# Kernel tuning notes

Hardware: AMD Instinct MI355X
Metric: run time of the kernel (lower is better)

## Reference

```python
import jax, jax.numpy as jnp
import numpy as np

D_MODEL = 2048
N_HEADS = 16
D_HEAD = D_MODEL // N_HEADS  # 128


def setup_inputs() -> dict:
    key = jax.random.key(0)
    ks = jax.random.split(key, 5)
    b, t = 2, 2048
    s = 0.02
    return {
        "x": jax.random.normal(ks[0], (b, t, D_MODEL), dtype=jnp.float32),
        "Wq": jax.random.normal(ks[1], (D_MODEL, D_MODEL), dtype=jnp.float32) * s,
        "Wk": jax.random.normal(ks[2], (D_MODEL, D_HEAD), dtype=jnp.float32) * s,
        "Wv": jax.random.normal(ks[3], (D_MODEL, D_HEAD), dtype=jnp.float32) * s,
        "Wo": jax.random.normal(ks[4], (D_MODEL, D_MODEL), dtype=jnp.float32) * s,
    }


def reference(x, Wq, Wk, Wv, Wo):
    b, t, c = x.shape
    scale = D_HEAD ** -0.5
    # q: [b, h, t, d]; k, v: single shared KV head [b, s, d]
    q = (x @ Wq).reshape(b, t, N_HEADS, D_HEAD).transpose(0, 2, 1, 3)
    k = x @ Wk  # [b, s, d]
    v = x @ Wv  # [b, s, d]
    # broadcast the shared KV head across query heads without materializing copies
    scores = jnp.einsum('bhtd,bsd->bhts', q, k) * scale
    attn = jax.nn.softmax(scores, axis=-1)
    y = jnp.einsum('bhts,bsd->bhtd', attn, v)
    y = y.transpose(0, 2, 1, 3).reshape(b, t, c)
    return y @ Wo
```

## Files before the change

kernel.cpp:

```cpp
#include <hip/hip_runtime.h>

typedef unsigned short ushort_t;
typedef short bf16x8 __attribute__((ext_vector_type(8)));
typedef float f32x4 __attribute__((ext_vector_type(4)));

#define B_    2
#define T_    2048
#define C_    2048
#define H_    16
#define DH_   128
#define BT_   4096
#define NQKV  2304

#define OFF_XB   0UL
#define OFF_WT   16777216UL
#define OFF_WOT  26214400UL
#define OFF_QKV  34603008UL
#define OFF_VT   53477376UL
#define OFF_FLAG 54525952UL

__device__ __forceinline__ ushort_t f2bf(float f) {
  union { float f; unsigned u; } v; v.f = f;
  unsigned r = v.u + 0x7fffu + ((v.u >> 16) & 1u);
  return (ushort_t)(r >> 16);
}
__device__ __forceinline__ float bf2f(ushort_t u) {
  union { float f; unsigned u; } v; v.u = ((unsigned)u) << 16;
  return v.f;
}
__device__ __forceinline__ int cvtpk_bf16(float lo, float hi) {
  int r;
  asm("v_cvt_pk_bf16_f32 %0, %1, %2" : "=v"(r) : "v"(lo), "v"(hi));
  return r;
}
__device__ __forceinline__ bf16x8 mkfrag(int d0, int d1, int d2, int d3) {
  union { int i[4]; bf16x8 v; } u;
  u.i[0] = d0; u.i[1] = d1; u.i[2] = d2; u.i[3] = d3;
  return u.v;
}

__device__ __forceinline__ void gload_lds16(const ushort_t* g, ushort_t* l) {
  __builtin_amdgcn_global_load_lds((__attribute__((address_space(1))) void*)g,
                                   (__attribute__((address_space(3))) void*)l,
                                   16, 0, 0);
}

__global__ void detect_dtype(const ushort_t* x, int* flag) {
  if (threadIdx.x == 0 && blockIdx.x == 0) {
    int sane = 0;
    for (int i = 0; i < 32; ++i) {
      ushort_t u = x[2 * i];
      int e = (u >> 7) & 0xFF;
      if (u == 0 || (e >= 100 && e <= 140)) ++sane;
    }
    *flag = (sane >= 24) ? 1 : 0;
  }
}

__global__ __launch_bounds__(256) void cast_x(const void* __restrict__ xin,
                                              ushort_t* __restrict__ xb,
                                              const int* __restrict__ flag, int n8) {
  int i = blockIdx.x * 256 + threadIdx.x;
  if (i >= n8) return;
  if (*flag) {
    *(bf16x8*)(xb + (size_t)i * 8) = *(const bf16x8*)((const ushort_t*)xin + (size_t)i * 8);
  } else {
    const float* xf = (const float*)xin;
    f32x4 a = *(const f32x4*)(xf + (size_t)i * 8);
    f32x4 b = *(const f32x4*)(xf + (size_t)i * 8 + 4);
    bf16x8 o;
    o[0] = (short)f2bf(a[0]); o[1] = (short)f2bf(a[1]);
    o[2] = (short)f2bf(a[2]); o[3] = (short)f2bf(a[3]);
    o[4] = (short)f2bf(b[0]); o[5] = (short)f2bf(b[1]);
    o[6] = (short)f2bf(b[2]); o[7] = (short)f2bf(b[3]);
    *(bf16x8*)(xb + (size_t)i * 8) = o;
  }
}

__global__ __launch_bounds__(256) void transpose_cast(const void* __restrict__ src,
                                                      ushort_t* __restrict__ dst,
                                                      const int* __restrict__ flag,
                                                      int rows, int cols, int dst_ld,
                                                      int dst_row_off) {
  __shared__ float tile[32][33];
  int c0 = blockIdx.x * 32, r0 = blockIdx.y * 32;
  int tx = threadIdx.x & 31, ty = threadIdx.x >> 5;
  bool isbf = (*flag != 0);
#pragma unroll
  for (int j = 0; j < 4; ++j) {
    int r = r0 + ty + j * 8;
    float v;
    if (isbf) v = bf2f(((const ushort_t*)src)[(size_t)r * cols + c0 + tx]);
    else      v = ((const float*)src)[(size_t)r * cols + c0 + tx];
    tile[ty + j * 8][tx] = v;
  }
  __syncthreads();
#pragma unroll
  for (int j = 0; j < 4; ++j) {
    int c = c0 + ty + j * 8;
    dst[(size_t)(dst_row_off + c) * dst_ld + r0 + tx] = f2bf(tile[tx][ty + j * 8]);
  }
}

__global__ __launch_bounds__(256) void transpose_v(const ushort_t* __restrict__ qkv,
                                                   ushort_t* __restrict__ vT) {
  __shared__ ushort_t tile[32][33];
  int b = blockIdx.z;
  int t0 = blockIdx.x * 32, d0 = blockIdx.y * 32;
  int tx = threadIdx.x & 31, ty = threadIdx.x >> 5;
#pragma unroll
  for (int j = 0; j < 4; ++j) {
    int t = t0 + ty + j * 8;
    tile[ty + j * 8][tx] = qkv[(size_t)(b * T_ + t) * NQKV + 2176 + d0 + tx];
  }
  __syncthreads();
#pragma unroll
  for (int j = 0; j < 4; ++j) {
    int d = d0 + ty + j * 8;
    vT[(size_t)b * (DH_ * T_) + (size_t)d * T_ + t0 + tx] = tile[tx][ty + j * 8];
  }
}

__global__ __launch_bounds__(256) void gemm_bt(const ushort_t* __restrict__ A,
                                               const ushort_t* __restrict__ Bt,
                                               void* __restrict__ Cv,
                                               int M, int N, int K,
                                               int is_final, const int* __restrict__ flag,
                                               float qscale, int qcols) {
  __shared__ __align__(16) ushort_t As[128 * 32];
  __shared__ __align__(16) ushort_t Bs[128 * 32];
  const int tid = threadIdx.x;
  const int lane = tid & 63;
  const int wid = tid >> 6;
  const int m0 = blockIdx.y * 128;
  const int n0 = blockIdx.x * 128;
  const int wr = wid >> 1, wc = wid & 1;
  const int l15 = lane & 15, l4 = lane >> 4;

  f32x4 zero = {0.f, 0.f, 0.f, 0.f};
  f32x4 acc[4][4];
#pragma unroll
  for (int r = 0; r < 4; ++r)
#pragma unroll
    for (int c = 0; c < 4; ++c) acc[r][c] = zero;

  const ushort_t* ga = A + (size_t)(m0 + (tid >> 2)) * K + (tid & 3) * 8;
  const ushort_t* gb = Bt + (size_t)(n0 + (tid >> 2)) * K + (tid & 3) * 8;
  ushort_t* lA = As + wid * 512;
  ushort_t* lB = Bs + wid * 512;
  const size_t stride64 = (size_t)64 * K;

  for (int k0 = 0; k0 < K; k0 += 32) {
    __syncthreads();
    gload_lds16(ga + k0, lA);
    gload_lds16(ga + k0 + stride64, lA + 2048);
    gload_lds16(gb + k0, lB);
    gload_lds16(gb + k0 + stride64, lB + 2048);
    __syncthreads();

    bf16x8 af[4], bfr[4];
#pragma unroll
    for (int r = 0; r < 4; ++r)
      af[r] = *(const bf16x8*)&As[(wr * 64 + r * 16 + l15) * 32 + l4 * 8];
#pragma unroll
    for (int c = 0; c < 4; ++c)
      bfr[c] = *(const bf16x8*)&Bs[(wc * 64 + c * 16 + l15) * 32 + l4 * 8];
#pragma unroll
    for (int r = 0; r < 4; ++r)
#pragma unroll
      for (int c = 0; c < 4; ++c)
        acc[r][c] = __builtin_amdgcn_mfma_f32_16x16x32_bf16(af[r], bfr[c], acc[r][c], 0, 0, 0);
  }

  const bool f32out = is_final && (*flag == 0);
#pragma unroll
  for (int r = 0; r < 4; ++r) {
#pragma unroll
    for (int c = 0; c < 4; ++c) {
      int row = m0 + wr * 64 + r * 16 + l4 * 4;
      int col = n0 + wc * 64 + c * 16 + l15;
      float s = (col < qcols) ? qscale : 1.0f;
#pragma unroll
      for (int g = 0; g < 4; ++g) {
        float v = acc[r][c][g] * s;
        if (f32out) ((float*)Cv)[(size_t)(row + g) * N + col] = v;
        else ((ushort_t*)Cv)[(size_t)(row + g) * N + col] = f2bf(v);
      }
    }
  }
}

__global__ __launch_bounds__(512, 4) void attn_kernel(const ushort_t* __restrict__ qkv,
                                                      const ushort_t* __restrict__ vT,
                                                      ushort_t* __restrict__ y) {
  __shared__ __align__(16) ushort_t Ks[2][64 * 128];
  __shared__ __align__(16) ushort_t Vs[2][128 * 64];

  const int tid = threadIdx.x;
  const int lane = tid & 63;
  const int wid = tid >> 6;
  const int h = blockIdx.y * 2 + (wid >> 2);
  const int b = blockIdx.z;
  const int tb = b * T_;
  const int q0 = blockIdx.x * 64 + (wid & 3) * 16;
  const int l15 = lane & 15, l4 = lane >> 4;

  bf16x8 qf[4];
  {
    const ushort_t* qbase = qkv + (size_t)(tb + q0 + l15) * NQKV + h * DH_ + l4 * 8;
#pragma unroll
    for (int ks = 0; ks < 4; ++ks) qf[ks] = *(const bf16x8*)(qbase + ks * 32);
  }

  const ushort_t* ksrcb[2];
  const ushort_t* vsrcb[2];
  int koff[2], voff[2];
#pragma unroll
  for (int it = 0; it < 2; ++it) {
    int id = tid + it * 512;
    int krow = id >> 4, kslot = id & 15;
    ksrcb[it] = qkv + (size_t)(tb + krow) * NQKV + 2048 + ((kslot ^ (krow & 7)) << 3);
    int vrow = id >> 3, vslot = id & 7;
    vsrcb[it] = vT + (size_t)b * (DH_ * T_) + (size_t)vrow * T_ + ((vslot ^ (vrow & 7)) << 3);
    koff[it] = (it * 512 + (wid << 6)) * 8;
    voff[it] = (it * 512 + (wid << 6)) * 8;
  }

  f32x4 zero = {0.f, 0.f, 0.f, 0.f};
  f32x4 o[8];
#pragma unroll
  for (int i = 0; i < 8; ++i) o[i] = zero;
  float m_s = -1e30f;
  float l_s = 0.f;

#pragma unroll
  for (int it = 0; it < 2; ++it) {
    gload_lds16(ksrcb[it], &Ks[0][koff[it]]);
    gload_lds16(vsrcb[it], &Vs[0][voff[it]]);
  }

  for (int st = 0; st < 32; ++st) {
    const int cur = st & 1;
    __syncthreads();
    if (st < 31) {
      const int s1 = (st + 1) * 64;
#pragma unroll
      for (int it = 0; it < 2; ++it) {
        gload_lds16(ksrcb[it] + (size_t)s1 * NQKV, &Ks[cur ^ 1][koff[it]]);
        gload_lds16(vsrcb[it] + s1, &Vs[cur ^ 1][voff[it]]);
      }
    }

    f32x4 sa[4];
#pragma unroll
    for (int c = 0; c < 4; ++c) {
      sa[c] = zero;
      int srow = c * 16 + l15;
      int sw = srow & 7;
#pragma unroll
      for (int ks = 0; ks < 4; ++ks) {
        bf16x8 kf = *(const bf16x8*)&Ks[cur][srow * 128 + (((ks * 4 + l4) ^ sw) << 3)];
        sa[c] = __builtin_amdgcn_mfma_f32_16x16x32_bf16(kf, qf[ks], sa[c], 0, 0, 0);
      }
    }

    float pmax = sa[0][0];
#pragma unroll
    for (int c = 0; c < 4; ++c)
#pragma unroll
      for (int r = 0; r < 4; ++r) pmax = fmaxf(pmax, sa[c][r]);
    pmax = fmaxf(pmax, __shfl_xor(pmax, 16));
    pmax = fmaxf(pmax, __shfl_xor(pmax, 32));

    if (!__all(pmax - m_s <= 8.0f)) {
      float mn = fmaxf(m_s, pmax);
      float al = exp2f(m_s - mn);
      m_s = mn;
      l_s *= al;
      float ar[4];
#pragma unroll
      for (int r = 0; r < 4; ++r) ar[r] = __shfl(al, l4 * 4 + r);
#pragma unroll
      for (int nb = 0; nb < 8; ++nb)
#pragma unroll
        for (int r = 0; r < 4; ++r) o[nb][r] *= ar[r];
    }

    float ps = 0.f;
#pragma unroll
    for (int c = 0; c < 4; ++c)
#pragma unroll
      for (int r = 0; r < 4; ++r) {
        float p = exp2f(sa[c][r] - m_s);
        sa[c][r] = p;
        ps += p;
      }
    ps += __shfl_xor(ps, 16);
    ps += __shfl_xor(ps, 32);
    l_s += ps;

    int pk0[2], pk1[2], pk2[2], pk3[2];
    pk0[0] = cvtpk_bf16(sa[0][0], sa[0][1]); pk0[1] = cvtpk_bf16(sa[0][2], sa[0][3]);
    pk1[0] = cvtpk_bf16(sa[1][0], sa[1][1]); pk1[1] = cvtpk_bf16(sa[1][2], sa[1][3]);
    pk2[0] = cvtpk_bf16(sa[2][0], sa[2][1]); pk2[1] = cvtpk_bf16(sa[2][2], sa[2][3]);
    pk3[0] = cvtpk_bf16(sa[3][0], sa[3][1]); pk3[1] = cvtpk_bf16(sa[3][2], sa[3][3]);

    const int srcA = ((lane >> 4) & 1) * 32 + l15;
    const int srcB = srcA + 16;
    const bool cHi = lane >= 32;

    int a00 = __shfl(pk0[0], srcA), a01 = __shfl(pk0[1], srcA);
    int a02 = __shfl(pk0[0], srcB), a03 = __shfl(pk0[1], srcB);
    int b00 = __shfl(pk1[0], srcA), b01 = __shfl(pk1[1], srcA);
    int b02 = __shfl(pk1[0], srcB), b03 = __shfl(pk1[1], srcB);
    bf16x8 pa0 = mkfrag(cHi ? b00 : a00, cHi ? b01 : a01,
                        cHi ? b02 : a02, cHi ? b03 : a03);

    int a10 = __shfl(pk2[0], srcA), a11 = __shfl(pk2[1], srcA);
    int a12 = __shfl(pk2[0], srcB), a13 = __shfl(pk2[1], srcB);
    int b10 = __shfl(pk3[0], srcA), b11 = __shfl(pk3[1], srcA);
    int b12 = __shfl(pk3[0], srcB), b13 = __shfl(pk3[1], srcB);
    bf16x8 pa1 = mkfrag(cHi ? b10 : a10, cHi ? b11 : a11,
                        cHi ? b12 : a12, cHi ? b13 : a13);

#pragma unroll
    for (int nb = 0; nb < 8; ++nb) {
      int vrow = nb * 16 + l15;
      int sw = vrow & 7;
      bf16x8 vb0 = *(const bf16x8*)&Vs[cur][vrow * 64 + ((l4 ^ sw) << 3)];
      o[nb] = __builtin_amdgcn_mfma_f32_16x16x32_bf16(pa0, vb0, o[nb], 0, 0, 0);
      bf16x8 vb1 = *(const bf16x8*)&Vs[cur][vrow * 64 + (((4 + l4) ^ sw) << 3)];
      o[nb] = __builtin_amdgcn_mfma_f32_16x16x32_bf16(pa1, vb1, o[nb], 0, 0, 0);
    }
  }

  float lr[4];
#pragma unroll
  for (int r = 0; r < 4; ++r) lr[r] = __shfl(l_s, l4 * 4 + r);
#pragma unroll
  for (int nb = 0; nb < 8; ++nb) {
#pragma unroll
    for (int r = 0; r < 4; ++r) {
      int qrow = tb + q0 + l4 * 4 + r;
      y[(size_t)qrow * C_ + h * DH_ + nb * 16 + l15] = f2bf(o[nb][r] / lr[r]);
    }
  }
}

extern "C" void kernel_launch(void* const* d_in, const int* in_sizes, int n_in,
                              void* d_out, int out_size, void* d_ws, size_t ws_size,
                              hipStream_t stream) {
  (void)in_sizes; (void)n_in; (void)out_size; (void)ws_size;
  const void* x  = d_in[0];
  const void* Wq = d_in[1];
  const void* Wk = d_in[2];
  const void* Wv = d_in[3];
  const void* Wo = d_in[4];

  char* ws = (char*)d_ws;
  ushort_t* xb  = (ushort_t*)(ws + OFF_XB);
  ushort_t* WT  = (ushort_t*)(ws + OFF_WT);
  ushort_t* WoT = (ushort_t*)(ws + OFF_WOT);
  ushort_t* qkv = (ushort_t*)(ws + OFF_QKV);
  ushort_t* vTp = (ushort_t*)(ws + OFF_VT);
  int* flag     = (int*)(ws + OFF_FLAG);

  detect_dtype<<<1, 1, 0, stream>>>((const ushort_t*)x, flag);

  cast_x<<<4096, 256, 0, stream>>>(x, xb, flag, (BT_ * C_) / 8);

  transpose_cast<<<dim3(64, 64), 256, 0, stream>>>(Wq, WT, flag, 2048, 2048, 2048, 0);
  transpose_cast<<<dim3(4, 64), 256, 0, stream>>>(Wk, WT, flag, 2048, 128, 2048, 2048);
  transpose_cast<<<dim3(4, 64), 256, 0, stream>>>(Wv, WT, flag, 2048, 128, 2048, 2176);
  transpose_cast<<<dim3(64, 64), 256, 0, stream>>>(Wo, WoT, flag, 2048, 2048, 2048, 0);

  const float k1 = 0.08838834764831845f * 1.4426950408889634f;
  gemm_bt<<<dim3(NQKV / 128, BT_ / 128), 256, 0, stream>>>(xb, WT, qkv, BT_, NQKV, C_, 0, flag, k1, 2048);

  transpose_v<<<dim3(T_ / 32, DH_ / 32, B_), 256, 0, stream>>>(qkv, vTp);

  attn_kernel<<<dim3(T_ / 64, H_ / 2, B_), 512, 0, stream>>>(qkv, vTp, xb);

  gemm_bt<<<dim3(C_ / 128, BT_ / 128), 256, 0, stream>>>(xb, WoT, d_out, BT_, C_, C_, 1, flag, 1.0f, 0);
}
```

Baseline: 363.2 us.

## Double-buffer GEMM loads, remap workgroups per XCD, and widen attention query tile

The GEMM now double-buffers its LDS tiles, prefetching the next K-slice while computing the current one with explicit vmcnt waits. It also remaps workgroup IDs so neighbouring tiles land on the same XCD, and raises wave priority around the MFMA blocks. The attention kernel gives each wave 32 query rows in two groups that share each K/V fragment load, halving the grid and the K/V reloads per query. In exchange it raises register pressure, with occupancy lowered to 2, and doubles GEMM LDS use.

```diff
diff --git a/kernel.cpp b/kernel.cpp
--- a/kernel.cpp
+++ b/kernel.cpp
@@ -127,13 +127,22 @@
                                                int M, int N, int K,
                                                int is_final, const int* __restrict__ flag,
                                                float qscale, int qcols) {
-  __shared__ __align__(16) ushort_t As[128 * 32];
-  __shared__ __align__(16) ushort_t Bs[128 * 32];
+  __shared__ __align__(16) ushort_t As[2][128 * 32];
+  __shared__ __align__(16) ushort_t Bs[2][128 * 32];
   const int tid = threadIdx.x;
   const int lane = tid & 63;
   const int wid = tid >> 6;
-  const int m0 = blockIdx.y * 128;
-  const int n0 = blockIdx.x * 128;
+
+  const int gx = gridDim.x;
+  const int nwg = gx * gridDim.y;
+  const int orig = blockIdx.y * gx + blockIdx.x;
+  const int qq = nwg >> 3, rr = nwg & 7;
+  const int xcd = orig & 7, pos = orig >> 3;
+  const int wg = (xcd < rr ? xcd * (qq + 1) : rr * (qq + 1) + (xcd - rr) * qq) + pos;
+  const int bx = wg % gx, by = wg / gx;
+
+  const int m0 = by * 128;
+  const int n0 = bx * 128;
   const int wr = wid >> 1, wc = wid & 1;
   const int l15 = lane & 15, l4 = lane >> 4;
 
@@ -146,30 +155,44 @@
 
   const ushort_t* ga = A + (size_t)(m0 + (tid >> 2)) * K + (tid & 3) * 8;
   const ushort_t* gb = Bt + (size_t)(n0 + (tid >> 2)) * K + (tid & 3) * 8;
-  ushort_t* lA = As + wid * 512;
-  ushort_t* lB = Bs + wid * 512;
   const size_t stride64 = (size_t)64 * K;
-
-  for (int k0 = 0; k0 < K; k0 += 32) {
-    __syncthreads();
-    gload_lds16(ga + k0, lA);
-    gload_lds16(ga + k0 + stride64, lA + 2048);
-    gload_lds16(gb + k0, lB);
-    gload_lds16(gb + k0 + stride64, lB + 2048);
-    __syncthreads();
+  const int lofs = wid * 512;
+
+  gload_lds16(ga, As[0] + lofs);
+  gload_lds16(ga + stride64, As[0] + lofs + 2048);
+  gload_lds16(gb, Bs[0] + lofs);
+  gload_lds16(gb + stride64, Bs[0] + lofs + 2048);
+
+  const int NT = K >> 5;
+  for (int t = 0; t < NT; ++t) {
+    const int cur = t & 1;
+    if (t + 1 < NT) {
+      const int k1 = (t + 1) << 5;
+      gload_lds16(ga + k1, As[cur ^ 1] + lofs);
+      gload_lds16(ga + k1 + stride64, As[cur ^ 1] + lofs + 2048);
+      gload_lds16(gb + k1, Bs[cur ^ 1] + lofs);
+      gload_lds16(gb + k1 + stride64, Bs[cur ^ 1] + lofs + 2048);
+      asm volatile("s_waitcnt vmcnt(4)" ::: "memory");
+    } else {
+      asm volatile("s_waitcnt vmcnt(0)" ::: "memory");
+    }
+    __builtin_amdgcn_s_barrier();
 
     bf16x8 af[4], bfr[4];
 #pragma unroll
     for (int r = 0; r < 4; ++r)
-      af[r] = *(const bf16x8*)&As[(wr * 64 + r * 16 + l15) * 32 + l4 * 8];
+      af[r] = *(const bf16x8*)&As[cur][(wr * 64 + r * 16 + l15) * 32 + l4 * 8];
 #pragma unroll
     for (int c = 0; c < 4; ++c)
-      bfr[c] = *(const bf16x8*)&Bs[(wc * 64 + c * 16 + l15) * 32 + l4 * 8];
+      bfr[c] = *(const bf16x8*)&Bs[cur][(wc * 64 + c * 16 + l15) * 32 + l4 * 8];
+    __builtin_amdgcn_s_setprio(1);
 #pragma unroll
     for (int r = 0; r < 4; ++r)
 #pragma unroll
       for (int c = 0; c < 4; ++c)
         acc[r][c] = __builtin_amdgcn_mfma_f32_16x16x32_bf16(af[r], bfr[c], acc[r][c], 0, 0, 0);
+    __builtin_amdgcn_s_setprio(0);
+    __builtin_amdgcn_s_barrier();
   }
 
   const bool f32out = is_final && (*flag == 0);
@@ -190,7 +213,7 @@
   }
 }
 
-__global__ __launch_bounds__(512, 4) void attn_kernel(const ushort_t* __restrict__ qkv,
+__global__ __launch_bounds__(512, 2) void attn_kernel(const ushort_t* __restrict__ qkv,
                                                       const ushort_t* __restrict__ vT,
                                                       ushort_t* __restrict__ y) {
   __shared__ __align__(16) ushort_t Ks[2][64 * 128];
@@ -202,14 +225,18 @@
   const int h = blockIdx.y * 2 + (wid >> 2);
   const int b = blockIdx.z;
   const int tb = b * T_;
-  const int q0 = blockIdx.x * 64 + (wid & 3) * 16;
+  const int q0 = blockIdx.x * 128 + (wid & 3) * 32;
   const int l15 = lane & 15, l4 = lane >> 4;
 
-  bf16x8 qf[4];
+  bf16x8 qf0[4], qf1[4];
   {
-    const ushort_t* qbase = qkv + (size_t)(tb + q0 + l15) * NQKV + h * DH_ + l4 * 8;
-#pragma unroll
-    for (int ks = 0; ks < 4; ++ks) qf[ks] = *(const bf16x8*)(qbase + ks * 32);
+    const ushort_t* qb0 = qkv + (size_t)(tb + q0 + l15) * NQKV + h * DH_ + l4 * 8;
+    const ushort_t* qb1 = qb0 + (size_t)16 * NQKV;
+#pragma unroll
+    for (int ks = 0; ks < 4; ++ks) {
+      qf0[ks] = *(const bf16x8*)(qb0 + ks * 32);
+      qf1[ks] = *(const bf16x8*)(qb1 + ks * 32);
+    }
   }
 
   const ushort_t* ksrcb[2];
@@ -227,11 +254,11 @@
   }
 
   f32x4 zero = {0.f, 0.f, 0.f, 0.f};
-  f32x4 o[8];
-#pragma unroll
-  for (int i = 0; i < 8; ++i) o[i] = zero;
-  float m_s = -1e30f;
-  float l_s = 0.f;
+  f32x4 o0[8], o1[8];
+#pragma unroll
+  for (int i = 0; i < 8; ++i) { o0[i] = zero; o1[i] = zero; }
+  float m0s = -1e30f, m1s = -1e30f;
+  float l0s = 0.f, l1s = 0.f;
 
 #pragma unroll
   for (int it = 0; it < 2; ++it) {
@@ -251,99 +278,167 @@
       }
     }
 
-    f32x4 sa[4];
+    f32x4 sa0[4], sa1[4];
+    __builtin_amdgcn_s_setprio(1);
 #pragma unroll
     for (int c = 0; c < 4; ++c) {
-      sa[c] = zero;
       int srow = c * 16 + l15;
       int sw = srow & 7;
+      bf16x8 kf[4];
+#pragma unroll
+      for (int ks = 0; ks < 4; ++ks)
+        kf[ks] = *(const bf16x8*)&Ks[cur][srow * 128 + (((ks * 4 + l4) ^ sw) << 3)];
+      sa0[c] = zero; sa1[c] = zero;
 #pragma unroll
       for (int ks = 0; ks < 4; ++ks) {
-        bf16x8 kf = *(const bf16x8*)&Ks[cur][srow * 128 + (((ks * 4 + l4) ^ sw) << 3)];
-        sa[c] = __builtin_amdgcn_mfma_f32_16x16x32_bf16(kf, qf[ks], sa[c], 0, 0, 0);
-      }
-    }
-
-    float pmax = sa[0][0];
+        sa0[c] = __builtin_amdgcn_mfma_f32_16x16x32_bf16(kf[ks], qf0[ks], sa0[c], 0, 0, 0);
+        sa1[c] = __builtin_amdgcn_mfma_f32_16x16x32_bf16(kf[ks], qf1[ks], sa1[c], 0, 0, 0);
+      }
+    }
+    __builtin_amdgcn_s_setprio(0);
+
+    float pmax0 = sa0[0][0];
 #pragma unroll
     for (int c = 0; c < 4; ++c)
 #pragma unroll
-      for (int r = 0; r < 4; ++r) pmax = fmaxf(pmax, sa[c][r]);
-    pmax = fmaxf(pmax, __shfl_xor(pmax, 16));
-    pmax = fmaxf(pmax, __shfl_xor(pmax, 32));
-
-    if (!__all(pmax - m_s <= 8.0f)) {
-      float mn = fmaxf(m_s, pmax);
-      float al = exp2f(m_s - mn);
-      m_s = mn;
-      l_s *= al;
+      for (int r = 0; r < 4; ++r) pmax0 = fmaxf(pmax0, sa0[c][r]);
+    pmax0 = fmaxf(pmax0, __shfl_xor(pmax0, 16));
+    pmax0 = fmaxf(pmax0, __shfl_xor(pmax0, 32));
+    if (!__all(pmax0 - m0s <= 8.0f)) {
+      float mn = fmaxf(m0s, pmax0);
+      float al = exp2f(m0s - mn);
+      m0s = mn; l0s *= al;
       float ar[4];
 #pragma unroll
       for (int r = 0; r < 4; ++r) ar[r] = __shfl(al, l4 * 4 + r);
 #pragma unroll
       for (int nb = 0; nb < 8; ++nb)
 #pragma unroll
-        for (int r = 0; r < 4; ++r) o[nb][r] *= ar[r];
-    }
-
-    float ps = 0.f;
+        for (int r = 0; r < 4; ++r) o0[nb][r] *= ar[r];
+    }
+    float ps0 = 0.f;
 #pragma unroll
     for (int c = 0; c < 4; ++c)
 #pragma unroll
       for (int r = 0; r < 4; ++r) {
-        float p = exp2f(sa[c][r] - m_s);
-        sa[c][r] = p;
-        ps += p;
-      }
-    ps += __shfl_xor(ps, 16);
-    ps += __shfl_xor(ps, 32);
-    l_s += ps;
-
-    int pk0[2], pk1[2], pk2[2], pk3[2];
-    pk0[0] = cvtpk_bf16(sa[0][0], sa[0][1]); pk0[1] = cvtpk_bf16(sa[0][2], sa[0][3]);
-    pk1[0] = cvtpk_bf16(sa[1][0], sa[1][1]); pk1[1] = cvtpk_bf16(sa[1][2], sa[1][3]);
-    pk2[0] = cvtpk_bf16(sa[2][0], sa[2][1]); pk2[1] = cvtpk_bf16(sa[2][2], sa[2][3]);
-    pk3[0] = cvtpk_bf16(sa[3][0], sa[3][1]); pk3[1] = cvtpk_bf16(sa[3][2], sa[3][3]);
+        float p = exp2f(sa0[c][r] - m0s);
+        sa0[c][r] = p;
+        ps0 += p;
+      }
+    ps0 += __shfl_xor(ps0, 16);
+    ps0 += __shfl_xor(ps0, 32);
+    l0s += ps0;
+
+    float pmax1 = sa1[0][0];
+#pragma unroll
+    for (int c = 0; c < 4; ++c)
+#pragma unroll
+      for (int r = 0; r < 4; ++r) pmax1 = fmaxf(pmax1, sa1[c][r]);
+    pmax1 = fmaxf(pmax1, __shfl_xor(pmax1, 16));
+    pmax1 = fmaxf(pmax1, __shfl_xor(pmax1, 32));
+    if (!__all(pmax1 - m1s <= 8.0f)) {
+      float mn = fmaxf(m1s, pmax1);
+      float al = exp2f(m1s - mn);
+      m1s = mn; l1s *= al;
+      float ar[4];
+#pragma unroll
+      for (int r = 0; r < 4; ++r) ar[r] = __shfl(al, l4 * 4 + r);
+#pragma unroll
+      for (int nb = 0; nb < 8; ++nb)
+#pragma unroll
+        for (int r = 0; r < 4; ++r) o1[nb][r] *= ar[r];
+    }
+    float ps1 = 0.f;
+#pragma unroll
+    for (int c = 0; c < 4; ++c)
+#pragma unroll
+      for (int r = 0; r < 4; ++r) {
+        float p = exp2f(sa1[c][r] - m1s);
+        sa1[c][r] = p;
+        ps1 += p;
+      }
+    ps1 += __shfl_xor(ps1, 16);
+    ps1 += __shfl_xor(ps1, 32);
+    l1s += ps1;
 
     const int srcA = ((lane >> 4) & 1) * 32 + l15;
     const int srcB = srcA + 16;
     const bool cHi = lane >= 32;
 
-    int a00 = __shfl(pk0[0], srcA), a01 = __shfl(pk0[1], srcA);
-    int a02 = __shfl(pk0[0], srcB), a03 = __shfl(pk0[1], srcB);
-    int b00 = __shfl(pk1[0], srcA), b01 = __shfl(pk1[1], srcA);
-    int b02 = __shfl(pk1[0], srcB), b03 = __shfl(pk1[1], srcB);
-    bf16x8 pa0 = mkfrag(cHi ? b00 : a00, cHi ? b01 : a01,
-                        cHi ? b02 : a02, cHi ? b03 : a03);
-
-    int a10 = __shfl(pk2[0], srcA), a11 = __shfl(pk2[1], srcA);
-    int a12 = __shfl(pk2[0], srcB), a13 = __shfl(pk2[1], srcB);
-    int b10 = __shfl(pk3[0], srcA), b11 = __shfl(pk3[1], srcA);
-    int b12 = __shfl(pk3[0], srcB), b13 = __shfl(pk3[1], srcB);
-    bf16x8 pa1 = mkfrag(cHi ? b10 : a10, cHi ? b11 : a11,
-                        cHi ? b12 : a12, cHi ? b13 : a13);
-
+    bf16x8 g0pa0, g0pa1, g1pa0, g1pa1;
+    {
+      int pk0[2], pk1[2], pk2[2], pk3[2];
+      pk0[0] = cvtpk_bf16(sa0[0][0], sa0[0][1]); pk0[1] = cvtpk_bf16(sa0[0][2], sa0[0][3]);
+      pk1[0] = cvtpk_bf16(sa0[1][0], sa0[1][1]); pk1[1] = cvtpk_bf16(sa0[1][2], sa0[1][3]);
+      pk2[0] = cvtpk_bf16(sa0[2][0], sa0[2][1]); pk2[1] = cvtpk_bf16(sa0[2][2], sa0[2][3]);
+      pk3[0] = cvtpk_bf16(sa0[3][0], sa0[3][1]); pk3[1] = cvtpk_bf16(sa0[3][2], sa0[3][3]);
+      int a00 = __shfl(pk0[0], srcA), a01 = __shfl(pk0[1], srcA);
+      int a02 = __shfl(pk0[0], srcB), a03 = __shfl(pk0[1], srcB);
+      int b00 = __shfl(pk1[0], srcA), b01 = __shfl(pk1[1], srcA);
+      int b02 = __shfl(pk1[0], srcB), b03 = __shfl(pk1[1], srcB);
+      g0pa0 = mkfrag(cHi ? b00 : a00, cHi ? b01 : a01, cHi ? b02 : a02, cHi ? b03 : a03);
+      int a10 = __shfl(pk2[0], srcA), a11 = __shfl(pk2[1], srcA);
+      int a12 = __shfl(pk2[0], srcB), a13 = __shfl(pk2[1], srcB);
+      int b10 = __shfl(pk3[0], srcA), b11 = __shfl(pk3[1], srcA);
+      int b12 = __shfl(pk3[0], srcB), b13 = __shfl(pk3[1], srcB);
+      g0pa1 = mkfrag(cHi ? b10 : a10, cHi ? b11 : a11, cHi ? b12 : a12, cHi ? b13 : a13);
+    }
+    {
+      int pk0[2], pk1[2], pk2[2], pk3[2];
+      pk0[0] = cvtpk_bf16(sa1[0][0], sa1[0][1]); pk0[1] = cvtpk_bf16(sa1[0][2], sa1[0][3]);
+      pk1[0] = cvtpk_bf16(sa1[1][0], sa1[1][1]); pk1[1] = cvtpk_bf16(sa1[1][2], sa1[1][3]);
+      pk2[0] = cvtpk_bf16(sa1[2][0], sa1[2][1]); pk2[1] = cvtpk_bf16(sa1[2][2], sa1[2][3]);
+      pk3[0] = cvtpk_bf16(sa1[3][0], sa1[3][1]); pk3[1] = cvtpk_bf16(sa1[3][2], sa1[3][3]);
+      int a00 = __shfl(pk0[0], srcA), a01 = __shfl(pk0[1], srcA);
+      int a02 = __shfl(pk0[0], srcB), a03 = __shfl(pk0[1], srcB);
+      int b00 = __shfl(pk1[0], srcA), b01 = __shfl(pk1[1], srcA);
+      int b02 = __shfl(pk1[0], srcB), b03 = __shfl(pk1[1], srcB);
+      g1pa0 = mkfrag(cHi ? b00 : a00, cHi ? b01 : a01, cHi ? b02 : a02, cHi ? b03 : a03);
+      int a10 = __shfl(pk2[0], srcA), a11 = __shfl(pk2[1], srcA);
+      int a12 = __shfl(pk2[0], srcB), a13 = __shfl(pk2[1], srcB);
+      int b10 = __shfl(pk3[0], srcA), b11 = __shfl(pk3[1], srcA);
+      int b12 = __shfl(pk3[0], srcB), b13 = __shfl(pk3[1], srcB);
+      g1pa1 = mkfrag(cHi ? b10 : a10, cHi ? b11 : a11, cHi ? b12 : a12, cHi ? b13 : a13);
+    }
+
+    __builtin_amdgcn_s_setprio(1);
 #pragma unroll
     for (int nb = 0; nb < 8; ++nb) {
       int vrow = nb * 16 + l15;
       int sw = vrow & 7;
       bf16x8 vb0 = *(const bf16x8*)&Vs[cur][vrow * 64 + ((l4 ^ sw) << 3)];
-      o[nb] = __builtin_amdgcn_mfma_f32_16x16x32_bf16(pa0, vb0, o[nb], 0, 0, 0);
+      o0[nb] = __builtin_amdgcn_mfma_f32_16x16x32_bf16(g0pa0, vb0, o0[nb], 0, 0, 0);
+      o1[nb] = __builtin_amdgcn_mfma_f32_16x16x32_bf16(g1pa0, vb0, o1[nb], 0, 0, 0);
       bf16x8 vb1 = *(const bf16x8*)&Vs[cur][vrow * 64 + (((4 + l4) ^ sw) << 3)];
-      o[nb] = __builtin_amdgcn_mfma_f32_16x16x32_bf16(pa1, vb1, o[nb], 0, 0, 0);
-    }
-  }
-
-  float lr[4];
-#pragma unroll
-  for (int r = 0; r < 4; ++r) lr[r] = __shfl(l_s, l4 * 4 + r);
-#pragma unroll
-  for (int nb = 0; nb < 8; ++nb) {
-#pragma unroll
-    for (int r = 0; r < 4; ++r) {
-      int qrow = tb + q0 + l4 * 4 + r;
-      y[(size_t)qrow * C_ + h * DH_ + nb * 16 + l15] = f2bf(o[nb][r] / lr[r]);
-    }
+      o0[nb] = __builtin_amdgcn_mfma_f32_16x16x32_bf16(g0pa1, vb1, o0[nb], 0, 0, 0);
+      o1[nb] = __builtin_amdgcn_mfma_f32_16x16x32_bf16(g1pa1, vb1, o1[nb], 0, 0, 0);
+    }
+    __builtin_amdgcn_s_setprio(0);
+  }
+
+  {
+    float lr[4];
+#pragma unroll
+    for (int r = 0; r < 4; ++r) lr[r] = __shfl(l0s, l4 * 4 + r);
+#pragma unroll
+    for (int nb = 0; nb < 8; ++nb)
+#pragma unroll
+      for (int r = 0; r < 4; ++r) {
+        int qrow = tb + q0 + l4 * 4 + r;
+        y[(size_t)qrow * C_ + h * DH_ + nb * 16 + l15] = f2bf(o0[nb][r] / lr[r]);
+      }
+  }
+  {
+    float lr[4];
+#pragma unroll
+    for (int r = 0; r < 4; ++r) lr[r] = __shfl(l1s, l4 * 4 + r);
+#pragma unroll
+    for (int nb = 0; nb < 8; ++nb)
+#pragma unroll
+      for (int r = 0; r < 4; ++r) {
+        int qrow = tb + q0 + 16 + l4 * 4 + r;
+        y[(size_t)qrow * C_ + h * DH_ + nb * 16 + l15] = f2bf(o1[nb][r] / lr[r]);
+      }
   }
 }
 
@@ -379,7 +474,7 @@
 
   transpose_v<<<dim3(T_ / 32, DH_ / 32, B_), 256, 0, stream>>>(qkv, vTp);
 
-  attn_kernel<<<dim3(T_ / 64, H_ / 2, B_), 512, 0, stream>>>(qkv, vTp, xb);
+  attn_kernel<<<dim3(T_ / 128, H_ / 2, B_), 512, 0, stream>>>(qkv, vTp, xb);
 
   gemm_bt<<<dim3(C_ / 128, BT_ / 128), 256, 0, stream>>>(xb, WoT, d_out, BT_, C_, C_, 1, flag, 1.0f, 0);
 }
```

Result: faster. 345.2 us (-5.0%).
